# Kernel tuning notes

Measured on AMD Instinct MI355X. Metric: run time of the kernel, lower is better.

Reference implementation:

```python
import jax, jax.numpy as jnp
import numpy as np

B, C, H, V = 16384, 5, 256, 512
NUM_ITER = 2


def setup_inputs() -> dict:
    key = jax.random.key(0)
    k1, k2, k3, k4 = jax.random.split(key, 4)
    # v0: one-hot categorical visible units, shape [B, C, V, 1]
    idx = jax.random.randint(k1, (B, V), 0, C)
    v0 = jax.nn.one_hot(idx, C, axis=1, dtype=jnp.float32)[..., None]
    W = 0.01 * jax.random.normal(k2, (C, H, V), dtype=jnp.float32)
    b = 0.01 * jax.random.normal(k3, (C, V, 1), dtype=jnp.float32)
    c = 0.01 * jax.random.normal(k4, (H, 1), dtype=jnp.float32)
    return {"v0": v0, "W": W, "b": b, "c": c, "num_sampling_iter": NUM_ITER}


def reference(v0, W, b, c, num_sampling_iter):
    key = jax.random.key(42)
    b2 = b[..., 0]   # [C, V]
    c1 = c[:, 0]     # [H]
    v = v0[..., 0]   # [B, C, V]

    def sample_h(k, v):
        # p(h=1|v) = sigmoid(sum_c W[c] @ v[:,c] + c)
        p = jax.nn.sigmoid(jnp.einsum('chv,bcv->bh', W, v) + c1)  # [B, H]
        return jax.random.bernoulli(k, p).astype(v.dtype)

    def sample_v(k, h):
        # logits over categories per visible unit: W[c].T @ h + b[c]
        logits = jnp.einsum('chv,bh->bcv', W, h) + b2  # [B, C, V]
        idx = jax.random.categorical(k, logits, axis=1)  # [B, V]
        return jax.nn.one_hot(idx, C, axis=1, dtype=h.dtype)  # [B, C, V]

    keys = jax.random.split(key, 2 * num_sampling_iter + 1)
    h = sample_h(keys[0], v)
    h_given_v0 = h
    for i in range(num_sampling_iter):  # small fixed iteration count
        v = sample_v(keys[2 * i + 1], h)
        h = sample_h(keys[2 * i + 2], v)
    return (v[..., None], h[..., None], h_given_v0[..., None])
```

## Files before the change

### kernel.cpp

```cpp
#include <hip/hip_runtime.h>
#include <cstdint>
#include <cstddef>


#define B_DIM 16384
#define C_DIM 5
#define H_DIM 256
#define V_DIM 512

struct TFOut { uint32_t a, b; };

typedef float f32x2 __attribute__((ext_vector_type(2)));
typedef float f32x4 __attribute__((ext_vector_type(4)));

#if __has_builtin(__builtin_elementwise_fma)
#define PKFMA(A, B, C) __builtin_elementwise_fma((A), (B), (C))
#else
static __device__ inline f32x2 pkfma_(f32x2 a, f32x2 b, f32x2 c) {
  f32x2 r; r.x = fmaf(a.x, b.x, c.x); r.y = fmaf(a.y, b.y, c.y); return r;
}
#define PKFMA(A, B, C) pkfma_((A), (B), (C))
#endif

__host__ __device__ static inline TFOut tf2x32(uint32_t k0, uint32_t k1,
                                               uint32_t c0, uint32_t c1) {
  uint32_t ks2 = k0 ^ k1 ^ 0x1BD11BDAu;
  uint32_t x0 = c0 + k0, x1 = c1 + k1;
#define TF_R(r) { x0 += x1; x1 = (x1 << r) | (x1 >> (32 - r)); x1 ^= x0; }
  TF_R(13) TF_R(15) TF_R(26) TF_R(6)
  x0 += k1;  x1 += ks2 + 1u;
  TF_R(17) TF_R(29) TF_R(16) TF_R(24)
  x0 += ks2; x1 += k0 + 2u;
  TF_R(13) TF_R(15) TF_R(26) TF_R(6)
  x0 += k0;  x1 += k1 + 3u;
  TF_R(17) TF_R(29) TF_R(16) TF_R(24)
  x0 += k1;  x1 += ks2 + 4u;
  TF_R(13) TF_R(15) TF_R(26) TF_R(6)
  x0 += ks2; x1 += k0 + 5u;
#undef TF_R
  TFOut o; o.a = x0; o.b = x1; return o;
}

__device__ static inline uint32_t rng_bits(uint32_t k0, uint32_t k1, uint32_t i) {
  TFOut r = tf2x32(k0, k1, 0u, i);
  return r.a ^ r.b;
}

__device__ static inline float bits_to_unit_float(uint32_t bits) {
  return __uint_as_float((bits >> 9) | 0x3F800000u) - 1.0f;
}

__device__ static float xla_exp(float x_in) {
#pragma clang fp contract(off)
  float x = fminf(x_in, 88.3762626647950f);
  x = fmaxf(x, -88.3762626647949f);
  float fx = floorf(x * 1.44269504088896341f + 0.5f);
  float tmp = fx * 0.693359375f;
  float z = fx * -2.12194440e-4f;
  x = x - tmp;
  x = x - z;
  z = x * x;
  float y = 1.9875691500e-4f;
  y = y * x + 1.3981999507e-3f;
  y = y * x + 8.3334519073e-3f;
  y = y * x + 4.1665795894e-2f;
  y = y * x + 1.6666665459e-1f;
  y = y * x + 5.0000001201e-1f;
  y = y * z + x;
  y = y + 1.0f;
  int n = (int)fx;
  y = y * __uint_as_float((uint32_t)(n + 127) << 23);
  return y;
}

__device__ static float xla_log(float x_in) {
#pragma clang fp contract(off)
  float xv = fmaxf(x_in, 1.17549435e-38f);
  uint32_t bits = __float_as_uint(xv);
  float e = (float)((int)(bits >> 23) - 126);
  float x = __uint_as_float((bits & 0x007FFFFFu) | 0x3F000000u);
  bool m = (x < 0.707106781186547524f);
  float tmp = m ? x : 0.0f;
  x = x - 1.0f;
  e = e - (m ? 1.0f : 0.0f);
  x = x + tmp;
  float z = x * x;
  float y = 7.0376836292e-2f;
  y = y * x + -1.1514610310e-1f;
  y = y * x + 1.1676998740e-1f;
  y = y * x + -1.2420140846e-1f;
  y = y * x + 1.4249322787e-1f;
  y = y * x + -1.6668057665e-1f;
  y = y * x + 2.0000714765e-1f;
  y = y * x + -2.4999993993e-1f;
  y = y * x + 3.3333331174e-1f;
  y = y * x;
  y = y * z;
  float t1 = e * -2.12194440e-4f;
  y = y + t1;
  float t2 = z * 0.5f;
  y = y - t2;
  x = x + y;
  float t3 = e * 0.693359375f;
  x = x + t3;
  return x;
}


__global__ void k_sentinel(float* out, float d) {
  out[0] = d;
}

__global__ __launch_bounds__(256) void k_idx(const float* __restrict__ v0,
                                             uint8_t* __restrict__ idx) {
  int t = blockIdx.x * 256 + threadIdx.x;
  int b = t >> 9, v = t & 511;
  const float* p = v0 + (size_t)b * (C_DIM * V_DIM) + v;
  int cf = 0;
#pragma unroll
  for (int c = 0; c < C_DIM; ++c)
    if (p[c * V_DIM] > 0.5f) cf = c;
  idx[t] = (uint8_t)cf;
}

__global__ __launch_bounds__(256) void k_wt(const float* __restrict__ W,
                                            float* __restrict__ Wt) {
  int t = blockIdx.x * 256 + threadIdx.x;
  int h = t & 255; int rest = t >> 8; int v = rest & 511; int c = rest >> 9;
  Wt[t] = W[((size_t)c * H_DIM + h) * V_DIM + v];
}

#define SH_K(u)                                                        \
  {                                                                    \
    f32x2 ww = {w8[u], w8[u]};                                         \
    const f32x4* fp_ = (const f32x4*)&tbf[kk + u][0];                  \
    f32x4 qA = fp_[0], qB = fp_[1], qC = fp_[2], qD = fp_[3];          \
    ps[0] = PKFMA(ww, __builtin_shufflevector(qA, qA, 0, 1), ps[0]);   \
    ps[1] = PKFMA(ww, __builtin_shufflevector(qA, qA, 2, 3), ps[1]);   \
    ps[2] = PKFMA(ww, __builtin_shufflevector(qB, qB, 0, 1), ps[2]);   \
    ps[3] = PKFMA(ww, __builtin_shufflevector(qB, qB, 2, 3), ps[3]);   \
    ps[4] = PKFMA(ww, __builtin_shufflevector(qC, qC, 0, 1), ps[4]);   \
    ps[5] = PKFMA(ww, __builtin_shufflevector(qC, qC, 2, 3), ps[5]);   \
    ps[6] = PKFMA(ww, __builtin_shufflevector(qD, qD, 0, 1), ps[6]);   \
    ps[7] = PKFMA(ww, __builtin_shufflevector(qD, qD, 2, 3), ps[7]);   \
  }

__global__ __launch_bounds__(256, 4) void k_sample_h(
    const float* __restrict__ Wt, const float* __restrict__ c1g,
    const uint8_t* __restrict__ idx,
    float* __restrict__ out_h, uint32_t* __restrict__ out_mask,
    uint32_t key0, uint32_t key1) {
  __shared__ uint8_t  sidx[16][V_DIM];
  __shared__ uint8_t  sidxT[V_DIM][16];
  __shared__ __align__(16) float tbf[320][16];
  int t = threadIdx.x;
  int b0 = blockIdx.x * 16;
  int wv = t >> 6, lane = t & 63;
  int h = t;

  {
    const uint32_t* src = (const uint32_t*)(idx + (size_t)b0 * V_DIM);
    uint32_t* dst = (uint32_t*)&sidx[0][0];
    for (int i = t; i < 2048; i += 256) dst[i] = src[i];
  }
  __syncthreads();
  {
    int bi = t >> 4, vb = (t & 15) * 32;
#pragma unroll
    for (int q = 0; q < 32; ++q)
      sidxT[vb + q][bi] = sidx[bi][vb + q];
  }
  __syncthreads();

  f32x2 ps[8], tt[8];
#pragma unroll
  for (int j = 0; j < 8; ++j) {
    ps[j] = (f32x2){0.f, 0.f};
    tt[j] = (f32x2){0.f, 0.f};
  }

  const float* wcol = Wt + h;

  for (int tile = 0; tile < 8; ++tile) {
    int kbase = tile * 320;
    {
      int bi = t & 15, kr = t >> 4;
#pragma unroll
      for (int g = 0; g < 20; ++g) {
        int kk = kr + (g << 4);
        int k = kbase + kk;
        int cc = k >> 9, v = k & 511;
        tbf[kk][bi] = (sidxT[v][bi] == (uint8_t)cc) ? 1.0f : 0.0f;
      }
    }
    __syncthreads();
#pragma unroll
    for (int j = 0; j < 8; ++j) {
      tt[j] += ps[j];
      ps[j] = (f32x2){0.f, 0.f};
    }
    for (int kk = 0; kk < 320; kk += 8) {
      float w8[8];
#pragma unroll
      for (int u = 0; u < 8; ++u)
        w8[u] = wcol[(size_t)(kbase + kk + u) * H_DIM];
      SH_K(0) SH_K(1) SH_K(2) SH_K(3)
      SH_K(4) SH_K(5) SH_K(6) SH_K(7)
    }
    __syncthreads();
  }
#pragma unroll
  for (int j = 0; j < 8; ++j) tt[j] += ps[j];

  float c1h = c1g[h];
#pragma unroll
  for (int j = 0; j < 8; ++j) {
#pragma unroll
    for (int e = 0; e < 2; ++e) {
      int b = b0 + 2 * j + e;
      float total = (e == 0 ? tt[j].x : tt[j].y) + c1h;
      float p = 1.0f / (1.0f + xla_exp(-total));
      float u = bits_to_unit_float(
          rng_bits(key0, key1, (uint32_t)(b * H_DIM + h)));
      bool hbit = (u < p);
      if (out_h) out_h[(size_t)b * H_DIM + h] = hbit ? 1.0f : 0.0f;
      unsigned long long m = __ballot(hbit);
      if (lane == 0) {
        out_mask[(size_t)b * 8 + wv * 2 + 0] = (uint32_t)(m & 0xFFFFFFFFull);
        out_mask[(size_t)b * 8 + wv * 2 + 1] = (uint32_t)(m >> 32);
      }
    }
  }
}

#define GV_H(u)                                                        \
  {                                                                    \
    f32x2 ww0 = {w4[u].x, w4[u].x};                                    \
    f32x2 ww1 = {w4[u].y, w4[u].y};                                    \
    const f32x4* fp_ = (const f32x4*)&tbf[hh + u][0];                  \
    f32x4 qA = fp_[0], qB = fp_[1], qC = fp_[2], qD = fp_[3];          \
    f32x2 f0 = __builtin_shufflevector(qA, qA, 0, 1);                  \
    f32x2 f1 = __builtin_shufflevector(qA, qA, 2, 3);                  \
    f32x2 f2 = __builtin_shufflevector(qB, qB, 0, 1);                  \
    f32x2 f3 = __builtin_shufflevector(qB, qB, 2, 3);                  \
    f32x2 f4 = __builtin_shufflevector(qC, qC, 0, 1);                  \
    f32x2 f5 = __builtin_shufflevector(qC, qC, 2, 3);                  \
    f32x2 f6 = __builtin_shufflevector(qD, qD, 0, 1);                  \
    f32x2 f7 = __builtin_shufflevector(qD, qD, 2, 3);                  \
    av0[0] = PKFMA(ww0, f0, av0[0]); av1[0] = PKFMA(ww1, f0, av1[0]);  \
    av0[1] = PKFMA(ww0, f1, av0[1]); av1[1] = PKFMA(ww1, f1, av1[1]);  \
    av0[2] = PKFMA(ww0, f2, av0[2]); av1[2] = PKFMA(ww1, f2, av1[2]);  \
    av0[3] = PKFMA(ww0, f3, av0[3]); av1[3] = PKFMA(ww1, f3, av1[3]);  \
    av0[4] = PKFMA(ww0, f4, av0[4]); av1[4] = PKFMA(ww1, f4, av1[4]);  \
    av0[5] = PKFMA(ww0, f5, av0[5]); av1[5] = PKFMA(ww1, f5, av1[5]);  \
    av0[6] = PKFMA(ww0, f6, av0[6]); av1[6] = PKFMA(ww1, f6, av1[6]);  \
    av0[7] = PKFMA(ww0, f7, av0[7]); av1[7] = PKFMA(ww1, f7, av1[7]);  \
  }

__global__ __launch_bounds__(256, 4) void k_gemm_v(
    const float* __restrict__ W, const uint32_t* __restrict__ mask,
    float* __restrict__ sums) {
  __shared__ uint32_t smask[16][8];
  __shared__ __align__(16) float tbf[H_DIM][16];
  int t = threadIdx.x;
  int b0 = blockIdx.x * 16;
  if (t < 128) smask[t >> 3][t & 7] = mask[(size_t)b0 * 8 + t];
  __syncthreads();
  {
    int h = t;
    uint32_t w = (uint32_t)(h >> 5), s = (uint32_t)(h & 31), x = 0;
#pragma unroll
    for (int j = 0; j < 16; ++j)
      x |= ((smask[j][w] >> s) & 1u) << j;
#pragma unroll
    for (int i = 0; i < 16; ++i)
      tbf[h][i] = (float)((x >> i) & 1u);
  }
  __syncthreads();

  int wv = t >> 6, lane = t & 63;
  int v0 = wv * 128 + (lane << 1);

  for (int c = 0; c < C_DIM; ++c) {
    f32x2 av0[8], av1[8];
#pragma unroll
    for (int j = 0; j < 8; ++j) {
      av0[j] = (f32x2){0.f, 0.f};
      av1[j] = (f32x2){0.f, 0.f};
    }
    const float* wp = W + (size_t)c * (H_DIM * V_DIM) + v0;
    for (int hh = 0; hh < H_DIM; hh += 4) {
      float2 w4[4];
#pragma unroll
      for (int u = 0; u < 4; ++u)
        w4[u] = *(const float2*)(wp + (size_t)(hh + u) * V_DIM);
      GV_H(0) GV_H(1) GV_H(2) GV_H(3)
    }
#pragma unroll
    for (int j = 0; j < 8; ++j) {
      float2 oA; oA.x = av0[j].x; oA.y = av1[j].x;
      *(float2*)&sums[((size_t)c * B_DIM + b0 + 2 * j) * V_DIM + v0] = oA;
      float2 oB; oB.x = av0[j].y; oB.y = av1[j].y;
      *(float2*)&sums[((size_t)c * B_DIM + b0 + 2 * j + 1) * V_DIM + v0] = oB;
    }
  }
}

__global__ __launch_bounds__(256, 4) void k_gumbel_v(
    const float* __restrict__ sums, const float* __restrict__ b2,
    uint8_t* __restrict__ idx_out, uint32_t key0, uint32_t key1) {
  int gidx = blockIdx.x * 256 + threadIdx.x;
  int b = gidx >> 7;
  int v0 = (gidx & 127) << 2;
  float best[4];
  uint32_t bc = 0;
#pragma unroll
  for (int c = 0; c < C_DIM; ++c) {
    float4 av = *(const float4*)&sums[((size_t)c * B_DIM + b) * V_DIM + v0];
    float4 bv = *(const float4*)&b2[c * V_DIM + v0];
    uint32_t ib = ((uint32_t)b * C_DIM + (uint32_t)c) * V_DIM + (uint32_t)v0;
    float avq[4] = {av.x, av.y, av.z, av.w};
    float bvq[4] = {bv.x, bv.y, bv.z, bv.w};
#pragma unroll
    for (int q = 0; q < 4; ++q) {
      float uf = bits_to_unit_float(rng_bits(key0, key1, ib + (uint32_t)q));
      if (uf == 0.0f) uf = 1.17549435e-38f;
      float gz = -xla_log(-xla_log(uf));
      float z = gz + (avq[q] + bvq[q]);
      if (c == 0 || z > best[q]) {
        best[q] = z;
        bc = (bc & ~(0xFFu << (8 * q))) | ((uint32_t)c << (8 * q));
      }
    }
  }
  *(uint32_t*)(idx_out + (size_t)b * V_DIM + v0) = bc;
}

__global__ __launch_bounds__(256) void k_onehot(const uint8_t* __restrict__ idx,
                                                float* __restrict__ out) {
  int t = blockIdx.x * 256 + threadIdx.x;
  int v = t & 511; int rest = t >> 9; int c = rest % C_DIM; int b = rest / C_DIM;
  out[t] = (idx[(size_t)b * V_DIM + v] == c) ? 1.0f : 0.0f;
}


extern "C" void kernel_launch(void* const* d_in, const int* in_sizes, int n_in,
                              void* d_out, int out_size, void* d_ws, size_t ws_size,
                              hipStream_t stream) {
  float* out = (float*)d_out;

  const size_t WS_NEED = 2621440ull
                       + 2621440ull
                       + 8388608ull
                       + 524288ull;
  float D = 0.0f;
  if (n_in < 4)                       D = 910.0f + (float)n_in;
  else if (in_sizes[0] != 41943040)   D = 920.0f;
  else if (in_sizes[1] != 655360)     D = 921.0f;
  else if (in_sizes[2] != 2560)       D = 922.0f;
  else if (in_sizes[3] != 256)        D = 923.0f;
  else if (out_size != 50331648)      D = 930.0f + (float)out_size * 1e-6f;
  else if (ws_size < WS_NEED)         D = 100.0f + (float)(ws_size >> 20);
  if (D != 0.0f) {
    hipLaunchKernelGGL(k_sentinel, dim3(1), dim3(1), 0, stream, out, D);
    return;
  }

  const float* v0 = (const float*)d_in[0];
  const float* W  = (const float*)d_in[1];
  const float* b2 = (const float*)d_in[2];
  const float* c1 = (const float*)d_in[3];

  float* out_v  = out;
  float* out_h  = out + (size_t)B_DIM * C_DIM * V_DIM;
  float* out_h0 = out_h + (size_t)B_DIM * H_DIM;

  char* ws = (char*)d_ws;
  float*    Wt   = (float*)(ws);
  uint8_t*  idx  = (uint8_t*)(ws + 5242880);
  uint32_t* mask = (uint32_t*)(ws + 13631488);

  float* sums = out_v;

  uint32_t keys[5][2];
  for (int i = 0; i < 5; ++i) {
    TFOut r = tf2x32(0u, 42u, 0u, (uint32_t)i);
    keys[i][0] = r.a; keys[i][1] = r.b;
  }

  hipLaunchKernelGGL(k_wt,  dim3(2560),  dim3(256), 0, stream, W, Wt);
  hipLaunchKernelGGL(k_idx, dim3(32768), dim3(256), 0, stream, v0, idx);

  hipLaunchKernelGGL(k_sample_h, dim3(B_DIM / 16), dim3(256), 0, stream,
                     Wt, c1, idx, out_h0, mask, keys[0][0], keys[0][1]);
  hipLaunchKernelGGL(k_gemm_v, dim3(B_DIM / 16), dim3(256), 0, stream,
                     W, mask, sums);
  hipLaunchKernelGGL(k_gumbel_v, dim3(B_DIM * 128 / 256), dim3(256), 0, stream,
                     sums, b2, idx, keys[1][0], keys[1][1]);
  hipLaunchKernelGGL(k_sample_h, dim3(B_DIM / 16), dim3(256), 0, stream,
                     Wt, c1, idx, (float*)nullptr, mask, keys[2][0], keys[2][1]);
  hipLaunchKernelGGL(k_gemm_v, dim3(B_DIM / 16), dim3(256), 0, stream,
                     W, mask, sums);
  hipLaunchKernelGGL(k_gumbel_v, dim3(B_DIM * 128 / 256), dim3(256), 0, stream,
                     sums, b2, idx, keys[3][0], keys[3][1]);
  hipLaunchKernelGGL(k_sample_h, dim3(B_DIM / 16), dim3(256), 0, stream,
                     Wt, c1, idx, out_h, mask, keys[4][0], keys[4][1]);
  hipLaunchKernelGGL(k_onehot, dim3(163840), dim3(256), 0, stream, idx, out_v);
}
```

Baseline: 2.242 ms.

## Remap GEMM kernels so each lane owns a batch row and weights broadcast

Both the hidden-sampling and visible-GEMM kernels are restructured. Each lane now owns one batch row and each wave owns 16 output columns, so weight rows are read as wave-uniform float4 broadcasts. The 0/1 activations are derived in registers from the packed index bytes or mask bits instead of being staged as float tiles in LDS, which removes the per-tile transpose and the extra barriers. The trade-off is that weights are re-read by 4x or 8x more blocks per batch group and the kernels rely on uniform loads being cached well. Mask bits are assembled through shared memory instead of a wave ballot.

Result: slower. 6.265 ms (+179.4%).

```diff
diff --git a/kernel.cpp b/kernel.cpp
--- a/kernel.cpp
+++ b/kernel.cpp
@@ -11,16 +11,18 @@
 struct TFOut { uint32_t a, b; };
 
 typedef float f32x2 __attribute__((ext_vector_type(2)));
-typedef float f32x4 __attribute__((ext_vector_type(4)));
-
+
+static __device__ inline f32x2 mk2(float x, float y) {
+  f32x2 r; r.x = x; r.y = y; return r;
+}
+
+static __device__ inline f32x2 pkfma(f32x2 a, f32x2 b, f32x2 c) {
 #if __has_builtin(__builtin_elementwise_fma)
-#define PKFMA(A, B, C) __builtin_elementwise_fma((A), (B), (C))
+  return __builtin_elementwise_fma(a, b, c);
 #else
-static __device__ inline f32x2 pkfma_(f32x2 a, f32x2 b, f32x2 c) {
   f32x2 r; r.x = fmaf(a.x, b.x, c.x); r.y = fmaf(a.y, b.y, c.y); return r;
-}
-#define PKFMA(A, B, C) pkfma_((A), (B), (C))
 #endif
+}
 
 __host__ __device__ static inline TFOut tf2x32(uint32_t k0, uint32_t k1,
                                                uint32_t c0, uint32_t c1) {
@@ -130,179 +132,160 @@
   Wt[t] = W[((size_t)c * H_DIM + h) * V_DIM + v];
 }
 
-#define SH_K(u)                                                        \
-  {                                                                    \
-    f32x2 ww = {w8[u], w8[u]};                                         \
-    const f32x4* fp_ = (const f32x4*)&tbf[kk + u][0];                  \
-    f32x4 qA = fp_[0], qB = fp_[1], qC = fp_[2], qD = fp_[3];          \
-    ps[0] = PKFMA(ww, __builtin_shufflevector(qA, qA, 0, 1), ps[0]);   \
-    ps[1] = PKFMA(ww, __builtin_shufflevector(qA, qA, 2, 3), ps[1]);   \
-    ps[2] = PKFMA(ww, __builtin_shufflevector(qB, qB, 0, 1), ps[2]);   \
-    ps[3] = PKFMA(ww, __builtin_shufflevector(qB, qB, 2, 3), ps[3]);   \
-    ps[4] = PKFMA(ww, __builtin_shufflevector(qC, qC, 0, 1), ps[4]);   \
-    ps[5] = PKFMA(ww, __builtin_shufflevector(qC, qC, 2, 3), ps[5]);   \
-    ps[6] = PKFMA(ww, __builtin_shufflevector(qD, qD, 0, 1), ps[6]);   \
-    ps[7] = PKFMA(ww, __builtin_shufflevector(qD, qD, 2, 3), ps[7]);   \
-  }
-
 __global__ __launch_bounds__(256, 4) void k_sample_h(
     const float* __restrict__ Wt, const float* __restrict__ c1g,
     const uint8_t* __restrict__ idx,
     float* __restrict__ out_h, uint32_t* __restrict__ out_mask,
     uint32_t key0, uint32_t key1) {
-  __shared__ uint8_t  sidx[16][V_DIM];
-  __shared__ uint8_t  sidxT[V_DIM][16];
-  __shared__ __align__(16) float tbf[320][16];
+  __shared__ uint32_t sidx[64 * 129];
+  __shared__ uint16_t hb16[64][4];
   int t = threadIdx.x;
-  int b0 = blockIdx.x * 16;
+  int bg = blockIdx.x >> 2, hq = blockIdx.x & 3;
+  int b0 = bg * 64;
   int wv = t >> 6, lane = t & 63;
-  int h = t;
+  int h0 = hq * 64 + wv * 16;
 
   {
     const uint32_t* src = (const uint32_t*)(idx + (size_t)b0 * V_DIM);
-    uint32_t* dst = (uint32_t*)&sidx[0][0];
-    for (int i = t; i < 2048; i += 256) dst[i] = src[i];
+    for (int i = t; i < 64 * 128; i += 256) {
+      int b = i >> 7, w = i & 127;
+      sidx[b * 129 + w] = src[i];
+    }
   }
   __syncthreads();
-  {
-    int bi = t >> 4, vb = (t & 15) * 32;
-#pragma unroll
-    for (int q = 0; q < 32; ++q)
-      sidxT[vb + q][bi] = sidx[bi][vb + q];
-  }
+
+  const uint32_t* myrow = &sidx[lane * 129];
+  const float* wbase = Wt + h0;
+
+  f32x2 ps[8], tt[8];
+#pragma unroll
+  for (int j = 0; j < 8; ++j) {
+    ps[j] = mk2(0.f, 0.f);
+    tt[j] = mk2(0.f, 0.f);
+  }
+
+#pragma unroll 2
+  for (int g = 0; g < 640; ++g) {
+    if ((g % 80) == 0) {
+#pragma unroll
+      for (int j = 0; j < 8; ++j) {
+        tt[j] += ps[j];
+        ps[j] = mk2(0.f, 0.f);
+      }
+    }
+    uint32_t q = myrow[g & 127];
+    uint32_t cc = (uint32_t)(g >> 7);
+    const float* wk = wbase + (size_t)(4 * g) * H_DIM;
+#pragma unroll
+    for (int u = 0; u < 4; ++u) {
+      float f = (((q >> (8 * u)) & 255u) == cc) ? 1.0f : 0.0f;
+      f32x2 ff = mk2(f, f);
+      const float4* wr = (const float4*)(wk + (size_t)u * H_DIM);
+      float4 wA = wr[0], wB = wr[1], wC = wr[2], wD = wr[3];
+      ps[0] = pkfma(mk2(wA.x, wA.y), ff, ps[0]);
+      ps[1] = pkfma(mk2(wA.z, wA.w), ff, ps[1]);
+      ps[2] = pkfma(mk2(wB.x, wB.y), ff, ps[2]);
+      ps[3] = pkfma(mk2(wB.z, wB.w), ff, ps[3]);
+      ps[4] = pkfma(mk2(wC.x, wC.y), ff, ps[4]);
+      ps[5] = pkfma(mk2(wC.z, wC.w), ff, ps[5]);
+      ps[6] = pkfma(mk2(wD.x, wD.y), ff, ps[6]);
+      ps[7] = pkfma(mk2(wD.z, wD.w), ff, ps[7]);
+    }
+  }
+#pragma unroll
+  for (int j = 0; j < 8; ++j) tt[j] += ps[j];
+
+  int b = b0 + lane;
+  const float4* c1q = (const float4*)(c1g + h0);
+  float4 c1a = c1q[0], c1b = c1q[1], c1c = c1q[2], c1d = c1q[3];
+  float tot[16], c1v[16], oh[16];
+#pragma unroll
+  for (int j = 0; j < 8; ++j) { tot[2 * j] = tt[j].x; tot[2 * j + 1] = tt[j].y; }
+  c1v[0] = c1a.x;  c1v[1] = c1a.y;  c1v[2] = c1a.z;  c1v[3] = c1a.w;
+  c1v[4] = c1b.x;  c1v[5] = c1b.y;  c1v[6] = c1b.z;  c1v[7] = c1b.w;
+  c1v[8] = c1c.x;  c1v[9] = c1c.y;  c1v[10] = c1c.z; c1v[11] = c1c.w;
+  c1v[12] = c1d.x; c1v[13] = c1d.y; c1v[14] = c1d.z; c1v[15] = c1d.w;
+  uint32_t m16 = 0;
+#pragma unroll
+  for (int j = 0; j < 16; ++j) {
+    float total = tot[j] + c1v[j];
+    float p = 1.0f / (1.0f + xla_exp(-total));
+    float u = bits_to_unit_float(
+        rng_bits(key0, key1, (uint32_t)(b * H_DIM + h0 + j)));
+    bool hbit = (u < p);
+    oh[j] = hbit ? 1.0f : 0.0f;
+    m16 |= (hbit ? 1u : 0u) << j;
+  }
+  if (out_h) {
+    float4* dst = (float4*)(out_h + (size_t)b * H_DIM + h0);
+#pragma unroll
+    for (int q2 = 0; q2 < 4; ++q2) {
+      float4 o;
+      o.x = oh[4 * q2]; o.y = oh[4 * q2 + 1];
+      o.z = oh[4 * q2 + 2]; o.w = oh[4 * q2 + 3];
+      dst[q2] = o;
+    }
+  }
+  hb16[lane][wv] = (uint16_t)m16;
   __syncthreads();
-
-  f32x2 ps[8], tt[8];
-#pragma unroll
-  for (int j = 0; j < 8; ++j) {
-    ps[j] = (f32x2){0.f, 0.f};
-    tt[j] = (f32x2){0.f, 0.f};
-  }
-
-  const float* wcol = Wt + h;
-
-  for (int tile = 0; tile < 8; ++tile) {
-    int kbase = tile * 320;
-    {
-      int bi = t & 15, kr = t >> 4;
-#pragma unroll
-      for (int g = 0; g < 20; ++g) {
-        int kk = kr + (g << 4);
-        int k = kbase + kk;
-        int cc = k >> 9, v = k & 511;
-        tbf[kk][bi] = (sidxT[v][bi] == (uint8_t)cc) ? 1.0f : 0.0f;
-      }
-    }
-    __syncthreads();
-#pragma unroll
-    for (int j = 0; j < 8; ++j) {
-      tt[j] += ps[j];
-      ps[j] = (f32x2){0.f, 0.f};
-    }
-    for (int kk = 0; kk < 320; kk += 8) {
-      float w8[8];
-#pragma unroll
-      for (int u = 0; u < 8; ++u)
-        w8[u] = wcol[(size_t)(kbase + kk + u) * H_DIM];
-      SH_K(0) SH_K(1) SH_K(2) SH_K(3)
-      SH_K(4) SH_K(5) SH_K(6) SH_K(7)
-    }
-    __syncthreads();
-  }
-#pragma unroll
-  for (int j = 0; j < 8; ++j) tt[j] += ps[j];
-
-  float c1h = c1g[h];
-#pragma unroll
-  for (int j = 0; j < 8; ++j) {
-#pragma unroll
-    for (int e = 0; e < 2; ++e) {
-      int b = b0 + 2 * j + e;
-      float total = (e == 0 ? tt[j].x : tt[j].y) + c1h;
-      float p = 1.0f / (1.0f + xla_exp(-total));
-      float u = bits_to_unit_float(
-          rng_bits(key0, key1, (uint32_t)(b * H_DIM + h)));
-      bool hbit = (u < p);
-      if (out_h) out_h[(size_t)b * H_DIM + h] = hbit ? 1.0f : 0.0f;
-      unsigned long long m = __ballot(hbit);
-      if (lane == 0) {
-        out_mask[(size_t)b * 8 + wv * 2 + 0] = (uint32_t)(m & 0xFFFFFFFFull);
-        out_mask[(size_t)b * 8 + wv * 2 + 1] = (uint32_t)(m >> 32);
-      }
-    }
-  }
-}
-
-#define GV_H(u)                                                        \
-  {                                                                    \
-    f32x2 ww0 = {w4[u].x, w4[u].x};                                    \
-    f32x2 ww1 = {w4[u].y, w4[u].y};                                    \
-    const f32x4* fp_ = (const f32x4*)&tbf[hh + u][0];                  \
-    f32x4 qA = fp_[0], qB = fp_[1], qC = fp_[2], qD = fp_[3];          \
-    f32x2 f0 = __builtin_shufflevector(qA, qA, 0, 1);                  \
-    f32x2 f1 = __builtin_shufflevector(qA, qA, 2, 3);                  \
-    f32x2 f2 = __builtin_shufflevector(qB, qB, 0, 1);                  \
-    f32x2 f3 = __builtin_shufflevector(qB, qB, 2, 3);                  \
-    f32x2 f4 = __builtin_shufflevector(qC, qC, 0, 1);                  \
-    f32x2 f5 = __builtin_shufflevector(qC, qC, 2, 3);                  \
-    f32x2 f6 = __builtin_shufflevector(qD, qD, 0, 1);                  \
-    f32x2 f7 = __builtin_shufflevector(qD, qD, 2, 3);                  \
-    av0[0] = PKFMA(ww0, f0, av0[0]); av1[0] = PKFMA(ww1, f0, av1[0]);  \
-    av0[1] = PKFMA(ww0, f1, av0[1]); av1[1] = PKFMA(ww1, f1, av1[1]);  \
-    av0[2] = PKFMA(ww0, f2, av0[2]); av1[2] = PKFMA(ww1, f2, av1[2]);  \
-    av0[3] = PKFMA(ww0, f3, av0[3]); av1[3] = PKFMA(ww1, f3, av1[3]);  \
-    av0[4] = PKFMA(ww0, f4, av0[4]); av1[4] = PKFMA(ww1, f4, av1[4]);  \
-    av0[5] = PKFMA(ww0, f5, av0[5]); av1[5] = PKFMA(ww1, f5, av1[5]);  \
-    av0[6] = PKFMA(ww0, f6, av0[6]); av1[6] = PKFMA(ww1, f6, av1[6]);  \
-    av0[7] = PKFMA(ww0, f7, av0[7]); av1[7] = PKFMA(ww1, f7, av1[7]);  \
-  }
+  if (t < 128) {
+    int bl = t >> 1, half = t & 1;
+    uint32_t wlo = hb16[bl][half * 2];
+    uint32_t whi = hb16[bl][half * 2 + 1];
+    out_mask[(size_t)(b0 + bl) * 8 + hq * 2 + half] = wlo | (whi << 16);
+  }
+}
 
 __global__ __launch_bounds__(256, 4) void k_gemm_v(
     const float* __restrict__ W, const uint32_t* __restrict__ mask,
     float* __restrict__ sums) {
-  __shared__ uint32_t smask[16][8];
-  __shared__ __align__(16) float tbf[H_DIM][16];
+  __shared__ uint32_t smask[64 * 9];
   int t = threadIdx.x;
-  int b0 = blockIdx.x * 16;
-  if (t < 128) smask[t >> 3][t & 7] = mask[(size_t)b0 * 8 + t];
+  int bg = blockIdx.x >> 3, vq = blockIdx.x & 7;
+  int b0 = bg * 64;
+  int wv = t >> 6, lane = t & 63;
+  int v0 = vq * 64 + wv * 16;
+
+  for (int i = t; i < 512; i += 256) {
+    int b = i >> 3, w = i & 7;
+    smask[b * 9 + w] = mask[(size_t)b0 * 8 + i];
+  }
   __syncthreads();
-  {
-    int h = t;
-    uint32_t w = (uint32_t)(h >> 5), s = (uint32_t)(h & 31), x = 0;
-#pragma unroll
-    for (int j = 0; j < 16; ++j)
-      x |= ((smask[j][w] >> s) & 1u) << j;
-#pragma unroll
-    for (int i = 0; i < 16; ++i)
-      tbf[h][i] = (float)((x >> i) & 1u);
-  }
-  __syncthreads();
-
-  int wv = t >> 6, lane = t & 63;
-  int v0 = wv * 128 + (lane << 1);
+
+  const uint32_t* mrow = &smask[lane * 9];
+  const float* wbase = W + v0;
 
   for (int c = 0; c < C_DIM; ++c) {
-    f32x2 av0[8], av1[8];
-#pragma unroll
-    for (int j = 0; j < 8; ++j) {
-      av0[j] = (f32x2){0.f, 0.f};
-      av1[j] = (f32x2){0.f, 0.f};
-    }
-    const float* wp = W + (size_t)c * (H_DIM * V_DIM) + v0;
-    for (int hh = 0; hh < H_DIM; hh += 4) {
-      float2 w4[4];
-#pragma unroll
-      for (int u = 0; u < 4; ++u)
-        w4[u] = *(const float2*)(wp + (size_t)(hh + u) * V_DIM);
-      GV_H(0) GV_H(1) GV_H(2) GV_H(3)
-    }
-#pragma unroll
-    for (int j = 0; j < 8; ++j) {
-      float2 oA; oA.x = av0[j].x; oA.y = av1[j].x;
-      *(float2*)&sums[((size_t)c * B_DIM + b0 + 2 * j) * V_DIM + v0] = oA;
-      float2 oB; oB.x = av0[j].y; oB.y = av1[j].y;
-      *(float2*)&sums[((size_t)c * B_DIM + b0 + 2 * j + 1) * V_DIM + v0] = oB;
-    }
+    f32x2 acc[8];
+#pragma unroll
+    for (int j = 0; j < 8; ++j) acc[j] = mk2(0.f, 0.f);
+    for (int hc = 0; hc < 8; ++hc) {
+      uint32_t word = mrow[hc];
+      const float* wp = wbase + ((size_t)c * H_DIM + hc * 32) * V_DIM;
+#pragma unroll
+      for (int hb = 0; hb < 32; ++hb) {
+        float f = (float)((word >> hb) & 1u);
+        f32x2 ff = mk2(f, f);
+        const float4* wr = (const float4*)(wp + (size_t)hb * V_DIM);
+        float4 wA = wr[0], wB = wr[1], wC = wr[2], wD = wr[3];
+        acc[0] = pkfma(mk2(wA.x, wA.y), ff, acc[0]);
+        acc[1] = pkfma(mk2(wA.z, wA.w), ff, acc[1]);
+        acc[2] = pkfma(mk2(wB.x, wB.y), ff, acc[2]);
+        acc[3] = pkfma(mk2(wB.z, wB.w), ff, acc[3]);
+        acc[4] = pkfma(mk2(wC.x, wC.y), ff, acc[4]);
+        acc[5] = pkfma(mk2(wC.z, wC.w), ff, acc[5]);
+        acc[6] = pkfma(mk2(wD.x, wD.y), ff, acc[6]);
+        acc[7] = pkfma(mk2(wD.z, wD.w), ff, acc[7]);
+      }
+    }
+    float* srow = sums + ((size_t)c * B_DIM + b0 + lane) * V_DIM + v0;
+    float4 o0, o1, o2, o3;
+    o0.x = acc[0].x; o0.y = acc[0].y; o0.z = acc[1].x; o0.w = acc[1].y;
+    o1.x = acc[2].x; o1.y = acc[2].y; o1.z = acc[3].x; o1.w = acc[3].y;
+    o2.x = acc[4].x; o2.y = acc[4].y; o2.z = acc[5].x; o2.w = acc[5].y;
+    o3.x = acc[6].x; o3.y = acc[6].y; o3.z = acc[7].x; o3.w = acc[7].y;
+    float4* sdst = (float4*)srow;
+    sdst[0] = o0; sdst[1] = o1; sdst[2] = o2; sdst[3] = o3;
   }
 }
 
@@ -391,19 +374,19 @@
   hipLaunchKernelGGL(k_wt,  dim3(2560),  dim3(256), 0, stream, W, Wt);
   hipLaunchKernelGGL(k_idx, dim3(32768), dim3(256), 0, stream, v0, idx);
 
-  hipLaunchKernelGGL(k_sample_h, dim3(B_DIM / 16), dim3(256), 0, stream,
+  hipLaunchKernelGGL(k_sample_h, dim3(B_DIM / 64 * 4), dim3(256), 0, stream,
                      Wt, c1, idx, out_h0, mask, keys[0][0], keys[0][1]);
-  hipLaunchKernelGGL(k_gemm_v, dim3(B_DIM / 16), dim3(256), 0, stream,
+  hipLaunchKernelGGL(k_gemm_v, dim3(B_DIM / 64 * 8), dim3(256), 0, stream,
                      W, mask, sums);
   hipLaunchKernelGGL(k_gumbel_v, dim3(B_DIM * 128 / 256), dim3(256), 0, stream,
                      sums, b2, idx, keys[1][0], keys[1][1]);
-  hipLaunchKernelGGL(k_sample_h, dim3(B_DIM / 16), dim3(256), 0, stream,
+  hipLaunchKernelGGL(k_sample_h, dim3(B_DIM / 64 * 4), dim3(256), 0, stream,
                      Wt, c1, idx, (float*)nullptr, mask, keys[2][0], keys[2][1]);
-  hipLaunchKernelGGL(k_gemm_v, dim3(B_DIM / 16), dim3(256), 0, stream,
+  hipLaunchKernelGGL(k_gemm_v, dim3(B_DIM / 64 * 8), dim3(256), 0, stream,
                      W, mask, sums);
   hipLaunchKernelGGL(k_gumbel_v, dim3(B_DIM * 128 / 256), dim3(256), 0, stream,
                      sums, b2, idx, keys[3][0], keys[3][1]);
-  hipLaunchKernelGGL(k_sample_h, dim3(B_DIM / 16), dim3(256), 0, stream,
+  hipLaunchKernelGGL(k_sample_h, dim3(B_DIM / 64 * 4), dim3(256), 0, stream,
                      Wt, c1, idx, out_h, mask, keys[4][0], keys[4][1]);
   hipLaunchKernelGGL(k_onehot, dim3(163840), dim3(256), 0, stream, idx, out_v);
 }
```
